# Performance work log

Measured on AMD Instinct MI355X. Metric: run time of the kernel, lower is better.

## Reference

```python
import jax, jax.numpy as jnp
import numpy as np

LN_EPS = 1e-5
NEG_SLOPE = 0.01  # torch LeakyReLU default


def layernorm(x, w, b):
    m = jnp.mean(x, axis=-1, keepdims=True)
    v = jnp.mean((x - m) ** 2, axis=-1, keepdims=True)
    return (x - m) * jax.lax.rsqrt(v + LN_EPS) * w + b


def setup_inputs() -> dict:
    key = jax.random.key(0)
    ks = jax.random.split(key, 12)
    B, T, C, E = 16, 1024, 768, 2
    d = C
    s = 0.02
    inp = {
        "x": jax.random.normal(ks[0], (B, T, C), jnp.float32),
        "ln1_w": jnp.ones((C,), jnp.float32),
        "ln1_b": jnp.zeros((C,), jnp.float32),
        "wqkv": jax.random.normal(ks[1], (C, 3 * C), jnp.float32) * s,
        "bqkv": jnp.zeros((3 * C,), jnp.float32),
        "wproj": jax.random.normal(ks[2], (C, C), jnp.float32) * s,
        "bproj": jnp.zeros((C,), jnp.float32),
        "ln2_w": jnp.ones((C,), jnp.float32),
        "ln2_b": jnp.zeros((C,), jnp.float32),
        "wg": jax.random.normal(ks[3], (C, E), jnp.float32) * s,
        # Experts module uses torch.randn (std 1); we scale down for numerics
        "w1": jax.random.normal(ks[4], (E, d, 4 * d), jnp.float32) * s,
        "w2": jax.random.normal(ks[5], (E, 4 * d, 4 * d), jnp.float32) * s,
        "w3": jax.random.normal(ks[6], (E, 4 * d, d), jnp.float32) * s,
        "n_head": 12,
    }
    return inp


def block_forward(x, ln1_w, ln1_b, wqkv, bqkv, wproj, bproj,
                  ln2_w, ln2_b, wg, w1, w2, w3, n_head):
    B, T, C = x.shape
    H = n_head
    hd = C // H
    E = wg.shape[-1]

    # ---- causal self-attention + residual ----
    h = layernorm(x, ln1_w, ln1_b)
    qkv = h @ wqkv + bqkv                      # [B,T,3C]
    q, k, v = jnp.split(qkv, 3, axis=-1)
    q = q.reshape(B, T, H, hd).transpose(0, 2, 1, 3)  # bhtd
    k = k.reshape(B, T, H, hd).transpose(0, 2, 1, 3)
    v = v.reshape(B, T, H, hd).transpose(0, 2, 1, 3)
    scores = jnp.einsum('bhqd,bhkd->bhqk', q, k) / jnp.sqrt(jnp.float32(hd))
    causal = jnp.tril(jnp.ones((T, T), bool))
    scores = jnp.where(causal, scores, jnp.finfo(scores.dtype).min)
    attn = jax.nn.softmax(scores, axis=-1)
    y = jnp.einsum('bhqk,bhkd->bhqd', attn, v)
    y = y.transpose(0, 2, 1, 3).reshape(B, T, C)
    x = x + (y @ wproj + bproj)

    # ---- MoE (top-2 gating, capacity dispatch) + residual ----
    h2 = layernorm(x, ln2_w, ln2_b)
    capacity = (T * 2) // E                    # capacity_factor = 1.0, top-2
    raw_gates = jax.nn.softmax(h2 @ wg, axis=-1)   # [B,T,E]

    idx1 = jnp.argmax(raw_gates, axis=-1)
    mask1 = jax.nn.one_hot(idx1, E, dtype=raw_gates.dtype)
    gate1 = jnp.sum(raw_gates * mask1, axis=-1)    # [B,T]
    gates2 = raw_gates * (1.0 - mask1)
    idx2 = jnp.argmax(gates2, axis=-1)
    mask2 = jax.nn.one_hot(idx2, E, dtype=raw_gates.dtype)
    gate2 = jnp.sum(raw_gates * mask2, axis=-1)
    denom = gate1 + gate2 + 1e-9
    gate1, gate2 = gate1 / denom, gate2 / denom

    # aux load-balancing loss (before capacity truncation)
    density = jnp.mean(mask1, axis=1)              # [B,E]
    density_proxy = jnp.mean(raw_gates, axis=1)    # [B,E]
    aux_loss = jnp.mean(density * density_proxy) * (E * E)

    # positions within each expert buffer (exclusive cumsum over tokens)
    pos1 = jnp.cumsum(mask1, axis=1) - mask1       # [B,T,E]
    mask1 = mask1 * (pos1 < capacity)
    mask1_count = jnp.sum(mask1, axis=1, keepdims=True)
    pos2 = (jnp.cumsum(mask2, axis=1) - mask2) + mask1_count
    mask2 = mask2 * (pos2 < capacity)

    oh1 = jax.nn.one_hot(pos1.astype(jnp.int32), capacity, dtype=raw_gates.dtype)
    oh2 = jax.nn.one_hot(pos2.astype(jnp.int32), capacity, dtype=raw_gates.dtype)
    combine = (gate1[..., None] * mask1)[..., None] * oh1 \
            + (gate2[..., None] * mask2)[..., None] * oh2   # [B,T,E,C]
    dispatch = (combine > 0).astype(h2.dtype)

    # dispatch -> per-expert batches
    expert_in = jnp.einsum('bnd,bnec->ebcd', h2, dispatch)   # [E,B,Cap,d]
    Bc = B * capacity
    ei = expert_in.reshape(E, Bc, C)
    lrelu = lambda z: jnp.where(z >= 0, z, NEG_SLOPE * z)
    hh = lrelu(jnp.einsum('end,edh->enh', ei, w1))
    hh = lrelu(jnp.einsum('end,edh->enh', hh, w2))
    eo = jnp.einsum('end,edh->enh', hh, w3).reshape(E, B, capacity, C)
    moe_out = jnp.einsum('ebcd,bnec->bnd', eo, combine)

    x = x + moe_out
    return x, aux_loss


def reference(x, ln1_w, ln1_b, wqkv, bqkv, wproj, bproj,
              ln2_w, ln2_b, wg, w1, w2, w3, n_head):
    return block_forward(x, ln1_w, ln1_b, wqkv, bqkv, wproj, bproj,
                         ln2_w, ln2_b, wg, w1, w2, w3, n_head)
```

## Files before the change

### kernel.cpp

```cpp
#include <hip/hip_runtime.h>
#include <cstdint>
#include <cstddef>

constexpr int B_  = 16;
constexpr int T_  = 1024;
constexpr int C_  = 768;
constexpr int H_  = 12;
constexpr int HD_ = 64;
constexpr int BT_ = B_ * T_;
constexpr int C3_ = 3 * C_;
constexpr int QK2_ = 2 * C_;
constexpr int FF_ = 4 * C_;
constexpr int MCH_ = 8192;

typedef __bf16 bf16x8 __attribute__((ext_vector_type(8)));
typedef float  floatx4 __attribute__((ext_vector_type(4)));
typedef unsigned short u16x8 __attribute__((ext_vector_type(8)));

__device__ inline float bf2f(unsigned short u) {
  union { unsigned int i; float f; } x; x.i = ((unsigned int)u) << 16; return x.f;
}
__device__ inline unsigned short f2bf(float f) {
  union { float f; unsigned int i; } x; x.f = f;
  unsigned int u = x.i;
  u += 0x7fffu + ((u >> 16) & 1u);
  return (unsigned short)(u >> 16);
}

#define GLOAD_LDS16(gp, lp)                                              \
  __builtin_amdgcn_global_load_lds(                                      \
      (__attribute__((address_space(1))) void*)(gp),                     \
      (__attribute__((address_space(3))) void*)(lp), 16, 0, 0)

__launch_bounds__(256)
__global__ void ln_kernel(const float* __restrict__ x, const float* __restrict__ w,
                          const float* __restrict__ b, unsigned short* __restrict__ out) {
  int row = blockIdx.x;
  int tid = threadIdx.x;
  const float* xr = x + (size_t)row * C_;
  float v0 = xr[tid], v1 = xr[tid + 256], v2 = xr[tid + 512];
  float s  = v0 + v1 + v2;
  float ss = v0 * v0 + v1 * v1 + v2 * v2;
#pragma unroll
  for (int off = 32; off > 0; off >>= 1) {
    s  += __shfl_down(s, off, 64);
    ss += __shfl_down(ss, off, 64);
  }
  __shared__ float red[8];
  int wid = tid >> 6;
  if ((tid & 63) == 0) { red[wid] = s; red[4 + wid] = ss; }
  __syncthreads();
  float st  = red[0] + red[1] + red[2] + red[3];
  float sst = red[4] + red[5] + red[6] + red[7];
  float mean = st * (1.0f / C_);
  float var  = sst * (1.0f / C_) - mean * mean;
  float rstd = rsqrtf(var + 1e-5f);
  unsigned short* orow = out + (size_t)row * C_;
  orow[tid]       = f2bf((v0 - mean) * rstd * w[tid]       + b[tid]);
  orow[tid + 256] = f2bf((v1 - mean) * rstd * w[tid + 256] + b[tid + 256]);
  orow[tid + 512] = f2bf((v2 - mean) * rstd * w[tid + 512] + b[tid + 512]);
}

struct CtJobs {
  const float* in[8];
  unsigned short* out[8];
  int K[8], N[8], tX[8];
  int t0[9];
};

__launch_bounds__(256)
__global__ void convT_batch(CtJobs J) {
  __shared__ float t[32][33];
  int bid = blockIdx.x;
  int ji = 0;
#pragma unroll
  for (int i = 0; i < 7; ++i) ji += (bid >= J.t0[i + 1]) ? 1 : 0;
  const float* in = J.in[ji];
  unsigned short* out = J.out[ji];
  const int K = J.K[ji], N = J.N[ji];
  const int lt = bid - J.t0[ji];
  const int bx = lt % J.tX[ji], by = lt / J.tX[ji];
  const int n0 = bx * 32, k0 = by * 32;
  const int tx = threadIdx.x & 31, ty = threadIdx.x >> 5;
#pragma unroll
  for (int r = 0; r < 32; r += 8)
    t[r + ty][tx] = in[(size_t)(k0 + r + ty) * N + n0 + tx];
  __syncthreads();
#pragma unroll
  for (int r = 0; r < 32; r += 8)
    out[(size_t)(n0 + r + ty) * K + k0 + tx] = f2bf(t[tx][r + ty]);
}

template <int ACT, bool BIAS, bool RES, bool COMBINE, bool OUTBF16,
          bool VSPLIT = false, bool ZB = false>
__launch_bounds__(256)
__global__ void gemm_bf16(const unsigned short* __restrict__ A,
                          const unsigned short* __restrict__ Bt,
                          const float* __restrict__ bias,
                          const float* __restrict__ Rres,
                          const float* __restrict__ gates2, int eidx,
                          void* __restrict__ Cout,
                          unsigned short* __restrict__ vtout,
                          int M, int N, int K,
                          size_t zsA, size_t zsB) {
  __shared__ __attribute__((aligned(16))) unsigned short Als[8192];
  __shared__ __attribute__((aligned(16))) unsigned short Bls[8192];
  const int tid  = threadIdx.x;
  const int wave = tid >> 6, lane = tid & 63;
  const int wr = wave >> 1, wc = wave & 1;

  if (ZB) {
    A  += (size_t)blockIdx.z * zsA;
    Bt += (size_t)blockIdx.z * zsB;
    eidx = (int)blockIdx.z;
  }

  int bx = blockIdx.x, by = blockIdx.y;
  {
    const int nbx = gridDim.x;
    const int nwg = nbx * gridDim.y;
    if ((nwg & 7) == 0) {
      const int bid = by * nbx + bx;
      const int swz = (bid & 7) * (nwg >> 3) + (bid >> 3);
      by = swz / nbx; bx = swz - by * nbx;
    }
  }
  const int m0 = by * 128, n0 = bx * 128;

  const int srow = wave * 32 + (lane >> 3);
  const int skg  = (lane & 7) ^ ((lane >> 3) & 7);
  const unsigned short* Ap = A  + (size_t)(m0 + srow) * K + skg * 8;
  const unsigned short* Bp = Bt + (size_t)(n0 + srow) * K + skg * 8;
  unsigned short* AlsW = Als + wave * 2048;
  unsigned short* BlsW = Bls + wave * 2048;

  floatx4 acc[4][4];
#pragma unroll
  for (int i = 0; i < 4; ++i)
#pragma unroll
    for (int j = 0; j < 4; ++j) acc[i][j] = floatx4{0.f, 0.f, 0.f, 0.f};

  const int q  = lane >> 4;
  const int ml = lane & 15;
  const int rsw = ml & 7;

  for (int k0 = 0; k0 < K; k0 += 64) {
    __syncthreads();
#pragma unroll
    for (int i = 0; i < 4; ++i) {
      GLOAD_LDS16(Ap + (size_t)(i * 8) * K + k0, AlsW + i * 512);
      GLOAD_LDS16(Bp + (size_t)(i * 8) * K + k0, BlsW + i * 512);
    }
    __syncthreads();
#pragma unroll
    for (int ks = 0; ks < 2; ++ks) {
      const int p = (ks * 4 + q) ^ rsw;
      bf16x8 af[4], bfg[4];
#pragma unroll
      for (int i = 0; i < 4; ++i) {
        int ar = wr * 64 + i * 16 + ml;
        af[i]  = *(const bf16x8*)&Als[(ar * 8 + p) * 8];
        int br = wc * 64 + i * 16 + ml;
        bfg[i] = *(const bf16x8*)&Bls[(br * 8 + p) * 8];
      }
#pragma unroll
      for (int i = 0; i < 4; ++i)
#pragma unroll
        for (int j = 0; j < 4; ++j)
          acc[i][j] = __builtin_amdgcn_mfma_f32_16x16x32_bf16(af[i], bfg[j], acc[i][j], 0, 0, 0);
    }
  }

  const int rbase = q * 4;
#pragma unroll
  for (int i = 0; i < 4; ++i) {
    int row = m0 + wr * 64 + i * 16 + rbase;
#pragma unroll
    for (int j = 0; j < 4; ++j) {
      int col = n0 + wc * 64 + j * 16 + ml;
      float bcol = BIAS ? bias[col] : 0.f;
#pragma unroll
      for (int r = 0; r < 4; ++r) {
        float v = acc[i][j][r];
        if (BIAS) v += bcol;
        if (ACT == 1) v = (v >= 0.f) ? v : 0.01f * v;
        if (RES) v += Rres[(size_t)(row + r) * N + col];
        if (COMBINE) {
          float g = gates2[2 * (row + r) + eidx];
          float* op = (float*)Cout + (size_t)(row + r) * N + col;
          if (ZB) atomicAdd(op, g * v);
          else    *op += g * v;
        } else if (VSPLIT) {
          if (col < QK2_) {
            ((unsigned short*)Cout)[(size_t)(row + r) * QK2_ + col] = f2bf(v);
          } else {
            vtout[(size_t)(col - QK2_) * BT_ + row + r] = f2bf(v);
          }
        } else if (OUTBF16) {
          ((unsigned short*)Cout)[(size_t)(row + r) * N + col] = f2bf(v);
        } else {
          ((float*)Cout)[(size_t)(row + r) * N + col] = v;
        }
      }
    }
  }
}

#define GB256_BAR()   asm volatile("s_barrier" ::: "memory")
#define GB256_LGKM0() asm volatile("s_waitcnt lgkmcnt(0)" ::: "memory")

template <int ACT, bool BIAS>
__launch_bounds__(512, 2)
__global__ void gemm256(const unsigned short* __restrict__ A,
                        const unsigned short* __restrict__ Bt,
                        const float* __restrict__ bias,
                        unsigned short* __restrict__ Cout,
                        int M, int N, int K,
                        size_t zsA, size_t zsB, size_t zsC) {
  __shared__ __attribute__((aligned(16))) unsigned short L[65536];
  const int tid = threadIdx.x;
  const int w = tid >> 6, l = tid & 63;
  const int wr = w >> 2, wc = w & 3;
  const int ml = l & 15, q = l >> 4;
  const int m0 = blockIdx.y * 256, n0 = blockIdx.x * 256;

  A    += (size_t)blockIdx.z * zsA;
  Bt   += (size_t)blockIdx.z * zsB;
  Cout += (size_t)blockIdx.z * zsC;

  const int srow = l >> 2;
  const int sg   = ((l & 3) ^ ((l >> 3) & 3)) * 8;
  const unsigned short* Ast = A  + (size_t)(m0 + srow) * K + sg;
  const unsigned short* Bst = Bt + (size_t)(n0 + srow) * K + sg;
  const int ldsw = w * 1024;

#define STG(cb, mat, ks, srcp, kk)                                           \
  do {                                                                       \
    const unsigned short* _s = (srcp) + (size_t)(w * 32) * K + (kk) + (ks) * 32; \
    unsigned short* _d = L + (cb) * 32768 + (mat) * 16384 + (ks) * 8192 + ldsw;  \
    GLOAD_LDS16(_s, _d);                                                     \
    GLOAD_LDS16(_s + (size_t)16 * K, _d + 512);                              \
  } while (0)

  const int dphys = (q ^ ((ml >> 1) & 3)) * 8;
  const int aoff = (wr * 128 + ml) * 32 + dphys;
  const int boff = (wc * 64 + ml) * 32 + dphys;

  floatx4 acc[8][4];
#pragma unroll
  for (int m = 0; m < 8; ++m)
#pragma unroll
    for (int n = 0; n < 4; ++n) acc[m][n] = floatx4{0.f, 0.f, 0.f, 0.f};

  const int NT = K >> 6;

  STG(0, 0, 0, Ast, 0);  STG(0, 1, 0, Bst, 0);
  STG(0, 0, 1, Ast, 0);  STG(0, 1, 1, Bst, 0);
  STG(1, 0, 0, Ast, 64); STG(1, 1, 0, Bst, 64);
  asm volatile("s_waitcnt vmcnt(0)" ::: "memory");
  GB256_BAR();

  for (int j = 0; j < NT; ++j) {
    const int c = j & 1, nx = c ^ 1;
    const int kk1 = (j + 1) << 6, kk2 = (j + 2) << 6;
    const bool st1 = (j + 1 < NT), st2 = (j + 2 < NT);
    bf16x8 bA[4], bB[4];

#define LOAD_A(KS, MH)                                                       \
  _Pragma("unroll")                                                          \
  for (int mq = 0; mq < 4; ++mq)                                             \
    bA[mq] = *(const bf16x8*)&L[c * 32768 + (KS) * 8192 + aoff + ((MH) * 4 + mq) * 512];
#define LOAD_B(KS)                                                           \
  _Pragma("unroll")                                                          \
  for (int n = 0; n < 4; ++n)                                                \
    bB[n] = *(const bf16x8*)&L[c * 32768 + 16384 + (KS) * 8192 + boff + n * 512];
#define MFMA16(MH)                                                           \
  __builtin_amdgcn_s_setprio(1);                                             \
  _Pragma("unroll")                                                          \
  for (int mq = 0; mq < 4; ++mq)                                             \
    _Pragma("unroll")                                                        \
    for (int n = 0; n < 4; ++n)                                              \
      acc[(MH) * 4 + mq][n] = __builtin_amdgcn_mfma_f32_16x16x32_bf16(       \
          bA[mq], bB[n], acc[(MH) * 4 + mq][n], 0, 0, 0);                    \
  __builtin_amdgcn_s_setprio(0);

    LOAD_B(0); LOAD_A(0, 0);
    if (st1) STG(nx, 0, 1, Ast, kk1);
    GB256_BAR(); GB256_LGKM0();
    MFMA16(0);
    GB256_BAR();

    LOAD_A(0, 1);
    if (st1) STG(nx, 1, 1, Bst, kk1);
    GB256_BAR(); GB256_LGKM0();
    MFMA16(1);
    GB256_BAR();

    LOAD_B(1); LOAD_A(1, 0);
    if (st2) STG(c, 0, 0, Ast, kk2);
    GB256_BAR(); GB256_LGKM0();
    MFMA16(0);
    GB256_BAR();

    LOAD_A(1, 1);
    if (st2) STG(c, 1, 0, Bst, kk2);
    GB256_BAR(); GB256_LGKM0();
    MFMA16(1);
    if (st2)      asm volatile("s_waitcnt vmcnt(4)" ::: "memory");
    else if (st1) asm volatile("s_waitcnt vmcnt(0)" ::: "memory");
    GB256_BAR();
#undef LOAD_A
#undef LOAD_B
#undef MFMA16
  }

#pragma unroll
  for (int m = 0; m < 8; ++m) {
    const int row = m0 + wr * 128 + m * 16 + q * 4;
#pragma unroll
    for (int n = 0; n < 4; ++n) {
      const int col = n0 + wc * 64 + n * 16 + ml;
      const float bcol = BIAS ? bias[col] : 0.f;
#pragma unroll
      for (int r = 0; r < 4; ++r) {
        float v = acc[m][n][r];
        if (BIAS) v += bcol;
        if (ACT == 1) v = (v >= 0.f) ? v : 0.01f * v;
        Cout[(size_t)(row + r) * N + col] = f2bf(v);
      }
    }
  }
#undef STG
}

__launch_bounds__(512)
__global__ void attn_kernel(const unsigned short* __restrict__ qk,
                            const unsigned short* __restrict__ vT,
                            unsigned short* __restrict__ y) {
  __shared__ __attribute__((aligned(16))) unsigned short Qls[128 * 64];
  __shared__ __attribute__((aligned(16))) unsigned short K2[2][64 * 64];
  __shared__ __attribute__((aligned(16))) unsigned short V2[2][64 * 64];
  __shared__ __attribute__((aligned(16))) unsigned short Pls[8 * 16 * 72];

  const int tid  = threadIdx.x;
  const int wave = tid >> 6, lane = tid & 63;
  const int quad = lane >> 4, n = lane & 15;
  const int q0 = blockIdx.x * 128;
  const int bh = blockIdx.y;
  const int b = bh / H_, h = bh % H_;
  const size_t qbase = (size_t)b * T_ * QK2_ + (size_t)h * HD_;
  const size_t vbase = (size_t)h * HD_ * BT_ + (size_t)b * T_;

  const int r8 = lane >> 3;
  const int g  = (lane & 7) ^ r8;

#pragma unroll
  for (int i = 0; i < 2; ++i) {
    int row = wave * 16 + i * 8 + r8;
    GLOAD_LDS16(qk + qbase + (size_t)(q0 + row) * QK2_ + g * 8,
                Qls + wave * 1024 + i * 512);
  }

#define STAGE_KV(bf, k0)                                                      \
  do {                                                                        \
    int row = wave * 8 + r8;                                                  \
    GLOAD_LDS16(qk + qbase + (size_t)((k0) + row) * QK2_ + C_ + g * 8,        \
                K2[bf] + wave * 512);                                         \
    GLOAD_LDS16(vT + vbase + (size_t)row * BT_ + (k0) + g * 8,                \
                V2[bf] + wave * 512);                                         \
  } while (0)

  STAGE_KV(0, 0);

  floatx4 O[4];
#pragma unroll
  for (int ct = 0; ct < 4; ++ct) O[ct] = floatx4{0.f, 0.f, 0.f, 0.f};
  float mrow[4] = {-1e30f, -1e30f, -1e30f, -1e30f};
  float lrow[4] = {0.f, 0.f, 0.f, 0.f};

  const int nkt = 2 * blockIdx.x + 2;
  const int dt  = 2 * blockIdx.x + (wave >> 2);
  unsigned short* Pw = Pls + wave * (16 * 72);

  for (int kt = 0; kt < nkt; ++kt) {
    const int cur = kt & 1;
    __syncthreads();
    if (kt + 1 < nkt) STAGE_KV(cur ^ 1, (kt + 1) << 6);
    if (kt > dt) continue;

    floatx4 sacc[4];
#pragma unroll
    for (int ct = 0; ct < 4; ++ct) sacc[ct] = floatx4{0.f, 0.f, 0.f, 0.f};
#pragma unroll
    for (int ks = 0; ks < 2; ++ks) {
      const int ga = (ks * 4 + quad) ^ (n & 7);
      bf16x8 aq = *(const bf16x8*)&Qls[((wave * 16 + n) * 8 + ga) * 8];
#pragma unroll
      for (int ct = 0; ct < 4; ++ct) {
        bf16x8 kb = *(const bf16x8*)&K2[cur][((ct * 16 + n) * 8 + ga) * 8];
        sacc[ct] = __builtin_amdgcn_mfma_f32_16x16x32_bf16(aq, kb, sacc[ct], 0, 0, 0);
      }
    }

    float p[4][4];
#pragma unroll
    for (int ct = 0; ct < 4; ++ct)
#pragma unroll
      for (int r = 0; r < 4; ++r) p[ct][r] = sacc[ct][r] * 0.125f;
    if (kt == dt) {
      const int kgb = (kt << 6) + n, qgb = q0 + wave * 16 + quad * 4;
#pragma unroll
      for (int ct = 0; ct < 4; ++ct)
#pragma unroll
        for (int r = 0; r < 4; ++r)
          if (kgb + ct * 16 > qgb + r) p[ct][r] = -1e30f;
    }
#pragma unroll
    for (int r = 0; r < 4; ++r) {
      float tm = fmaxf(fmaxf(p[0][r], p[1][r]), fmaxf(p[2][r], p[3][r]));
      tm = fmaxf(tm, __shfl_xor(tm, 1, 64));
      tm = fmaxf(tm, __shfl_xor(tm, 2, 64));
      tm = fmaxf(tm, __shfl_xor(tm, 4, 64));
      tm = fmaxf(tm, __shfl_xor(tm, 8, 64));
      float mn = fmaxf(mrow[r], tm);
      float alpha = __expf(mrow[r] - mn);
      mrow[r] = mn;
      float ps = 0.f;
#pragma unroll
      for (int ct = 0; ct < 4; ++ct) {
        float pe = __expf(p[ct][r] - mn);
        p[ct][r] = pe;
        ps += pe;
      }
      ps += __shfl_xor(ps, 1, 64);
      ps += __shfl_xor(ps, 2, 64);
      ps += __shfl_xor(ps, 4, 64);
      ps += __shfl_xor(ps, 8, 64);
      lrow[r] = lrow[r] * alpha + ps;
      O[0][r] *= alpha; O[1][r] *= alpha; O[2][r] *= alpha; O[3][r] *= alpha;
    }

#pragma unroll
    for (int ct = 0; ct < 4; ++ct)
#pragma unroll
      for (int r = 0; r < 4; ++r)
        Pw[(quad * 4 + r) * 72 + ct * 16 + n] = f2bf(p[ct][r]);

#pragma unroll
    for (int ks = 0; ks < 2; ++ks) {
      bf16x8 pa = *(const bf16x8*)&Pw[n * 72 + (ks * 4 + quad) * 8];
      const int gv = (ks * 4 + quad) ^ (n & 7);
#pragma unroll
      for (int ct = 0; ct < 4; ++ct) {
        bf16x8 vb = *(const bf16x8*)&V2[cur][((ct * 16 + n) * 8 + gv) * 8];
        O[ct] = __builtin_amdgcn_mfma_f32_16x16x32_bf16(pa, vb, O[ct], 0, 0, 0);
      }
    }
  }

#pragma unroll
  for (int r = 0; r < 4; ++r) {
    float inv = 1.0f / lrow[r];
    int row = q0 + wave * 16 + quad * 4 + r;
    unsigned short* dst = y + ((size_t)b * T_ + row) * C_ + h * HD_;
#pragma unroll
    for (int ct = 0; ct < 4; ++ct)
      dst[ct * 16 + n] = f2bf(O[ct][r] * inv);
  }
#undef STAGE_KV
}

__launch_bounds__(256)
__global__ void gate_kernel(const unsigned short* __restrict__ h2,
                            const float* __restrict__ wg,
                            float* __restrict__ gates) {
  int wave = threadIdx.x >> 6, lane = threadIdx.x & 63;
  int t = blockIdx.x * 4 + wave;
  const unsigned short* hr = h2 + (size_t)t * C_;
  float a0 = 0.0f, a1 = 0.0f;
#pragma unroll
  for (int i = 0; i < 12; ++i) {
    int d = lane + 64 * i;
    float hv = bf2f(hr[d]);
    a0 += hv * wg[2 * d];
    a1 += hv * wg[2 * d + 1];
  }
#pragma unroll
  for (int off = 32; off > 0; off >>= 1) {
    a0 += __shfl_down(a0, off, 64);
    a1 += __shfl_down(a1, off, 64);
  }
  if (lane == 0) {
    float m  = fmaxf(a0, a1);
    float e0 = __expf(a0 - m), e1 = __expf(a1 - m);
    float invs = 1.0f / (e0 + e1);
    float p0 = e0 * invs, p1 = e1 * invs;
    const float gnorm = 1.0f / (1.0f + 1e-9f);
    gates[2 * t]     = p0 * gnorm;
    gates[2 * t + 1] = p1 * gnorm;
  }
}

__launch_bounds__(1024)
__global__ void moe_stats_kernel(const float* __restrict__ gates,
                                 float* __restrict__ out_aux) {
  int wave = threadIdx.x >> 6, lane = threadIdx.x & 63;
  float c0 = 0.f, sp0 = 0.f, sp1 = 0.f;
#pragma unroll
  for (int j = 0; j < 16; ++j) {
    int t = wave * T_ + lane + 64 * j;
    float p0 = gates[2 * t], p1 = gates[2 * t + 1];
    c0  += (p1 > p0) ? 0.f : 1.f;
    sp0 += p0;
    sp1 += p1;
  }
#pragma unroll
  for (int off = 32; off > 0; off >>= 1) {
    c0  += __shfl_down(c0, off, 64);
    sp0 += __shfl_down(sp0, off, 64);
    sp1 += __shfl_down(sp1, off, 64);
  }
  __shared__ float red[16][3];
  if (lane == 0) { red[wave][0] = c0; red[wave][1] = sp0; red[wave][2] = sp1; }
  __syncthreads();
  if (threadIdx.x == 0) {
    float s = 0.f;
    for (int b = 0; b < B_; ++b) {
      float cc0 = red[b][0];
      float d0 = cc0 * (1.f / T_), d1 = (T_ - cc0) * (1.f / T_);
      float px0 = red[b][1] * (1.f / T_), px1 = red[b][2] * (1.f / T_);
      s += d0 * px0 + d1 * px1;
    }
    out_aux[0] = s * (4.f / 32.f);
  }
}

extern "C" void kernel_launch(void* const* d_in, const int* in_sizes, int n_in,
                              void* d_out, int out_size, void* d_ws, size_t ws_size,
                              hipStream_t stream) {
  const float* x     = (const float*)d_in[0];
  const float* ln1_w = (const float*)d_in[1];
  const float* ln1_b = (const float*)d_in[2];
  const float* wqkv  = (const float*)d_in[3];
  const float* bqkv  = (const float*)d_in[4];
  const float* wproj = (const float*)d_in[5];
  const float* bproj = (const float*)d_in[6];
  const float* ln2_w = (const float*)d_in[7];
  const float* ln2_b = (const float*)d_in[8];
  const float* wg    = (const float*)d_in[9];
  const float* w1    = (const float*)d_in[10];
  const float* w2    = (const float*)d_in[11];
  const float* w3    = (const float*)d_in[12];
  float* out = (float*)d_out;

  unsigned short* wsu   = (unsigned short*)d_ws;
  unsigned short* wqkvT = wsu;
  unsigned short* wprojT= wqkvT + (size_t)C3_ * C_;
  unsigned short* w1T   = wprojT + (size_t)C_ * C_;
  unsigned short* w2T   = w1T + (size_t)2 * FF_ * C_;
  unsigned short* w3T   = w2T + (size_t)2 * FF_ * FF_;
  unsigned short* hb    = w3T + (size_t)2 * C_ * FF_;
  unsigned short* region= hb + (size_t)BT_ * C_;
  unsigned short* qkb   = region;
  unsigned short* vTb   = region + (size_t)BT_ * QK2_;
  unsigned short* yb    = region + (size_t)BT_ * 3 * C_;

  const size_t regionElems = (size_t)BT_ * 4 * C_;
  const size_t bigElems    = (size_t)4 * MCH_ * FF_;
  const size_t baseElems   = (size_t)(region - wsu);
  const bool   big = ws_size >= (baseElems + bigElems + 65536) * sizeof(unsigned short);

  float* gates = (float*)(region + (big ? bigElems : regionElems));

  {
    CtJobs J;
    int idx = 0, acc = 0;
    auto add = [&](const float* in, unsigned short* outp, int K, int N) {
      J.in[idx] = in; J.out[idx] = outp; J.K[idx] = K; J.N[idx] = N;
      J.tX[idx] = N / 32; J.t0[idx] = acc;
      acc += (N / 32) * (K / 32);
      ++idx;
    };
    add(wqkv, wqkvT, C_, C3_);
    add(wproj, wprojT, C_, C_);
    for (int e = 0; e < 2; ++e) {
      add(w1 + (size_t)e * C_ * FF_, w1T + (size_t)e * FF_ * C_, C_, FF_);
      add(w2 + (size_t)e * FF_ * FF_, w2T + (size_t)e * FF_ * FF_, FF_, FF_);
      add(w3 + (size_t)e * FF_ * C_, w3T + (size_t)e * C_ * FF_, FF_, C_);
    }
    J.t0[8] = acc;
    convT_batch<<<acc, 256, 0, stream>>>(J);
  }

  ln_kernel<<<BT_, 256, 0, stream>>>(x, ln1_w, ln1_b, hb);
  gemm_bf16<0, true, false, false, true, true><<<dim3(C3_ / 128, BT_ / 128), 256, 0, stream>>>(
      hb, wqkvT, bqkv, nullptr, nullptr, 0, qkb, vTb, BT_, C3_, C_, 0, 0);
  attn_kernel<<<dim3(T_ / 128, B_ * H_), 512, 0, stream>>>(qkb, vTb, yb);
  gemm_bf16<0, true, true, false, false><<<dim3(C_ / 128, BT_ / 128), 256, 0, stream>>>(
      yb, wprojT, bproj, x, nullptr, 0, out, nullptr, BT_, C_, C_, 0, 0);

  ln_kernel<<<BT_, 256, 0, stream>>>(out, ln2_w, ln2_b, hb);
  gate_kernel<<<BT_ / 4, 256, 0, stream>>>(hb, wg, gates);
  moe_stats_kernel<<<1, 1024, 0, stream>>>(gates, out + (size_t)BT_ * C_);

  if (big) {
    unsigned short* hh1b = region;
    unsigned short* hh2b = region + (size_t)2 * MCH_ * FF_;
    for (int c = 0; c < BT_ / MCH_; ++c) {
      const unsigned short* a = hb + (size_t)c * MCH_ * C_;
      gemm256<1, false><<<dim3(FF_ / 256, MCH_ / 256, 2), 512, 0, stream>>>(
          a, w1T, nullptr, hh1b, MCH_, FF_, C_,
          0, (size_t)FF_ * C_, (size_t)MCH_ * FF_);
      gemm256<1, false><<<dim3(FF_ / 256, MCH_ / 256, 2), 512, 0, stream>>>(
          hh1b, w2T, nullptr, hh2b, MCH_, FF_, FF_,
          (size_t)MCH_ * FF_, (size_t)FF_ * FF_, (size_t)MCH_ * FF_);
      gemm_bf16<0, false, false, true, false, false, true>
          <<<dim3(C_ / 128, MCH_ / 128, 2), 256, 0, stream>>>(
          hh2b, w3T, nullptr, nullptr,
          gates + (size_t)2 * c * MCH_, 0, out + (size_t)c * MCH_ * C_, nullptr,
          MCH_, C_, FF_, (size_t)MCH_ * FF_, (size_t)C_ * FF_);
    }
  } else {
    unsigned short* hh1 = region;
    unsigned short* hh2 = region + (size_t)MCH_ * FF_;
    for (int e = 0; e < 2; ++e) {
      for (int c = 0; c < BT_ / MCH_; ++c) {
        const unsigned short* a = hb + (size_t)c * MCH_ * C_;
        gemm_bf16<1, false, false, false, true><<<dim3(FF_ / 128, MCH_ / 128), 256, 0, stream>>>(
            a, w1T + (size_t)e * FF_ * C_, nullptr, nullptr, nullptr, 0, hh1, nullptr,
            MCH_, FF_, C_, 0, 0);
        gemm_bf16<1, false, false, false, true><<<dim3(FF_ / 128, MCH_ / 128), 256, 0, stream>>>(
            hh1, w2T + (size_t)e * FF_ * FF_, nullptr, nullptr, nullptr, 0, hh2, nullptr,
            MCH_, FF_, FF_, 0, 0);
        gemm_bf16<0, false, false, true, false><<<dim3(C_ / 128, MCH_ / 128), 256, 0, stream>>>(
            hh2, w3T + (size_t)e * C_ * FF_, nullptr, nullptr,
            gates + (size_t)2 * c * MCH_, e, out + (size_t)c * MCH_ * C_, nullptr,
            MCH_, C_, FF_, 0, 0);
      }
    }
  }
}
```

Before: 1.586 ms.

## Fuse gating into second layernorm and swizzle gemm256 block order

The gate projection and softmax now run inside the second layernorm kernel, using the fp32 normalized values, so the separate gate kernel launch and its re-read of the bf16 activations go away. Separately, gemm256 remaps block indices with a stride-8 swizzle so that blocks scheduled together touch different tiles, which is aimed at L2 locality across chiplets. Gate logits are now computed from fp32 values rather than bf16-rounded ones, which can change top-1 choices slightly near ties.

Measured after the change: 1.593 ms. No clear change (+0.4%).

```diff
diff --git a/kernel.cpp b/kernel.cpp
--- a/kernel.cpp
+++ b/kernel.cpp
@@ -32,9 +32,11 @@
       (__attribute__((address_space(1))) void*)(gp),                     \
       (__attribute__((address_space(3))) void*)(lp), 16, 0, 0)
 
+template <bool GATE>
 __launch_bounds__(256)
 __global__ void ln_kernel(const float* __restrict__ x, const float* __restrict__ w,
-                          const float* __restrict__ b, unsigned short* __restrict__ out) {
+                          const float* __restrict__ b, unsigned short* __restrict__ out,
+                          const float* __restrict__ wg, float* __restrict__ gates) {
   int row = blockIdx.x;
   int tid = threadIdx.x;
   const float* xr = x + (size_t)row * C_;
@@ -55,10 +57,36 @@
   float mean = st * (1.0f / C_);
   float var  = sst * (1.0f / C_) - mean * mean;
   float rstd = rsqrtf(var + 1e-5f);
+  float h0 = (v0 - mean) * rstd * w[tid]       + b[tid];
+  float h1 = (v1 - mean) * rstd * w[tid + 256] + b[tid + 256];
+  float h2 = (v2 - mean) * rstd * w[tid + 512] + b[tid + 512];
   unsigned short* orow = out + (size_t)row * C_;
-  orow[tid]       = f2bf((v0 - mean) * rstd * w[tid]       + b[tid]);
-  orow[tid + 256] = f2bf((v1 - mean) * rstd * w[tid + 256] + b[tid + 256]);
-  orow[tid + 512] = f2bf((v2 - mean) * rstd * w[tid + 512] + b[tid + 512]);
+  orow[tid]       = f2bf(h0);
+  orow[tid + 256] = f2bf(h1);
+  orow[tid + 512] = f2bf(h2);
+
+  if (GATE) {
+    float a0 = h0 * wg[2 * tid]     + h1 * wg[2 * (tid + 256)]     + h2 * wg[2 * (tid + 512)];
+    float a1 = h0 * wg[2 * tid + 1] + h1 * wg[2 * (tid + 256) + 1] + h2 * wg[2 * (tid + 512) + 1];
+#pragma unroll
+    for (int off = 32; off > 0; off >>= 1) {
+      a0 += __shfl_down(a0, off, 64);
+      a1 += __shfl_down(a1, off, 64);
+    }
+    __shared__ float redg[8];
+    if ((tid & 63) == 0) { redg[wid] = a0; redg[4 + wid] = a1; }
+    __syncthreads();
+    if (tid == 0) {
+      float A0 = redg[0] + redg[1] + redg[2] + redg[3];
+      float A1 = redg[4] + redg[5] + redg[6] + redg[7];
+      float m  = fmaxf(A0, A1);
+      float e0 = __expf(A0 - m), e1 = __expf(A1 - m);
+      float invs = 1.0f / (e0 + e1);
+      const float gnorm = 1.0f / (1.0f + 1e-9f);
+      gates[2 * row]     = e0 * invs * gnorm;
+      gates[2 * row + 1] = e1 * invs * gnorm;
+    }
+  }
 }
 
 struct CtJobs {
@@ -222,11 +250,22 @@
   const int w = tid >> 6, l = tid & 63;
   const int wr = w >> 2, wc = w & 3;
   const int ml = l & 15, q = l >> 4;
-  const int m0 = blockIdx.y * 256, n0 = blockIdx.x * 256;
 
   A    += (size_t)blockIdx.z * zsA;
   Bt   += (size_t)blockIdx.z * zsB;
   Cout += (size_t)blockIdx.z * zsC;
+
+  int bx = blockIdx.x, by = blockIdx.y;
+  {
+    const int nbx = gridDim.x;
+    const int nwg = nbx * gridDim.y;
+    if ((nwg & 7) == 0) {
+      const int bid = by * nbx + bx;
+      const int swz = (bid & 7) * (nwg >> 3) + (bid >> 3);
+      by = swz / nbx; bx = swz - by * nbx;
+    }
+  }
+  const int m0 = by * 256, n0 = bx * 256;
 
   const int srow = l >> 2;
   const int sg   = ((l & 3) ^ ((l >> 3) & 3)) * 8;
@@ -470,37 +509,6 @@
 #undef STAGE_KV
 }
 
-__launch_bounds__(256)
-__global__ void gate_kernel(const unsigned short* __restrict__ h2,
-                            const float* __restrict__ wg,
-                            float* __restrict__ gates) {
-  int wave = threadIdx.x >> 6, lane = threadIdx.x & 63;
-  int t = blockIdx.x * 4 + wave;
-  const unsigned short* hr = h2 + (size_t)t * C_;
-  float a0 = 0.0f, a1 = 0.0f;
-#pragma unroll
-  for (int i = 0; i < 12; ++i) {
-    int d = lane + 64 * i;
-    float hv = bf2f(hr[d]);
-    a0 += hv * wg[2 * d];
-    a1 += hv * wg[2 * d + 1];
-  }
-#pragma unroll
-  for (int off = 32; off > 0; off >>= 1) {
-    a0 += __shfl_down(a0, off, 64);
-    a1 += __shfl_down(a1, off, 64);
-  }
-  if (lane == 0) {
-    float m  = fmaxf(a0, a1);
-    float e0 = __expf(a0 - m), e1 = __expf(a1 - m);
-    float invs = 1.0f / (e0 + e1);
-    float p0 = e0 * invs, p1 = e1 * invs;
-    const float gnorm = 1.0f / (1.0f + 1e-9f);
-    gates[2 * t]     = p0 * gnorm;
-    gates[2 * t + 1] = p1 * gnorm;
-  }
-}
-
 __launch_bounds__(1024)
 __global__ void moe_stats_kernel(const float* __restrict__ gates,
                                  float* __restrict__ out_aux) {
@@ -592,15 +600,14 @@
     convT_batch<<<acc, 256, 0, stream>>>(J);
   }
 
-  ln_kernel<<<BT_, 256, 0, stream>>>(x, ln1_w, ln1_b, hb);
+  ln_kernel<false><<<BT_, 256, 0, stream>>>(x, ln1_w, ln1_b, hb, nullptr, nullptr);
   gemm_bf16<0, true, false, false, true, true><<<dim3(C3_ / 128, BT_ / 128), 256, 0, stream>>>(
       hb, wqkvT, bqkv, nullptr, nullptr, 0, qkb, vTb, BT_, C3_, C_, 0, 0);
   attn_kernel<<<dim3(T_ / 128, B_ * H_), 512, 0, stream>>>(qkb, vTb, yb);
   gemm_bf16<0, true, true, false, false><<<dim3(C_ / 128, BT_ / 128), 256, 0, stream>>>(
       yb, wprojT, bproj, x, nullptr, 0, out, nullptr, BT_, C_, C_, 0, 0);
 
-  ln_kernel<<<BT_, 256, 0, stream>>>(out, ln2_w, ln2_b, hb);
-  gate_kernel<<<BT_ / 4, 256, 0, stream>>>(hb, wg, gates);
+  ln_kernel<true><<<BT_, 256, 0, stream>>>(out, ln2_w, ln2_b, hb, wg, gates);
   moe_stats_kernel<<<1, 1024, 0, stream>>>(gates, out + (size_t)BT_ * C_);
 
   if (big) {
```
